# Optimization experiments

Hardware: AMD Instinct MI355X
Metric: run time of the kernel (lower is better)

The kernel has to match this reference:

```python
import jax, jax.numpy as jnp
import numpy as np
from jax import lax

WEIGHT_PREC = 8
ACT_PREC = 8
ACT_BOUND = 6.0  # fixed symmetric activation bound (quant_act.bounds)
EPS = 1e-6


def _ste_round(v):
    # AQT round-to-nearest with straight-through estimator
    return v + lax.stop_gradient(jnp.floor(v + 0.5) - v)


def setup_inputs() -> dict:
    key = jax.random.key(0)
    k1, k2 = jax.random.split(key)
    B, D, F = 131072, 512, 512
    x = jax.random.normal(k1, (B, D), dtype=jnp.float32)
    # lecun_normal-style kernel init
    kernel = jax.random.normal(k2, (D, F), dtype=jnp.float32) * (1.0 / np.sqrt(D))
    bias = jnp.zeros((F,), dtype=jnp.float32)
    padding_mask = jnp.ones((B, 1), dtype=bool)
    return {"x": x, "kernel": kernel, "bias": bias, "padding_mask": padding_mask}


def reference(x, kernel, bias, padding_mask):
    # padding_mask only affects bounds statistics collection; with fixed act
    # bounds and train=False it does not enter the math.
    wmax = float(2 ** (WEIGHT_PREC - 1) - 1)  # 127
    amax = float(2 ** (ACT_PREC - 1) - 1)     # 127

    # per-channel weight quantization: axis=(0,), scale shape (1, features)
    w_bound = jnp.maximum(jnp.max(jnp.abs(kernel), axis=0, keepdims=True), EPS)
    w_scale = wmax / w_bound                   # (1, F)
    w_q = jnp.clip(_ste_round(kernel * w_scale), -wmax, wmax)

    # per-tensor symmetric activation quantization with fixed bound
    a_scale = amax / ACT_BOUND                 # scalar
    x_q = jnp.clip(_ste_round(x * a_scale), -amax, amax)

    # integer-valued dot_general, then dequantize by the combined scale
    y = jnp.einsum('bd,df->bf', x_q, w_q)      # [B, F]
    y = y / (a_scale * w_scale)                # broadcast (1, F)
    return y + bias[jnp.newaxis, :]
```

## Files before the change

kernel.cpp:

```cpp
#include <hip/hip_runtime.h>
#include <stdint.h>

typedef int   int32x4   __attribute__((ext_vector_type(4)));
typedef int   int32x16  __attribute__((ext_vector_type(16)));
typedef float floatx4   __attribute__((ext_vector_type(4)));

#define B_ROWS 131072
#define DK 512
#define FN 512
#define A_SCALE_F ((float)(127.0 / 6.0))

#define GBLK 256
#define GT   512
#define BMS  32
#define GTILES (B_ROWS / BMS / GBLK)

__global__ void wq_quant_kernel(const float* __restrict__ kern,
                                int8_t* __restrict__ wq,
                                float* __restrict__ invcs) {
  __shared__ float smax[256];
  __shared__ float sscale[4];
  const int c = threadIdx.x & 3;
  const int g = threadIdx.x >> 2;
  const int col = blockIdx.x * 4 + c;

  float m = 0.f;
#pragma unroll
  for (int i = 0; i < 8; ++i) {
    m = fmaxf(m, fabsf(kern[(size_t)(g * 8 + i) * FN + col]));
  }
  smax[threadIdx.x] = m;
  __syncthreads();
  if (threadIdx.x < 4) {
    float mm = smax[threadIdx.x];
#pragma unroll 8
    for (int g2 = 1; g2 < 64; ++g2) mm = fmaxf(mm, smax[g2 * 4 + threadIdx.x]);
    const float wb = fmaxf(mm, 1e-6f);
    const float ws = 127.f / wb;
    sscale[threadIdx.x] = ws;
    invcs[blockIdx.x * 4 + threadIdx.x] =
        (float)(1.0 / ((double)A_SCALE_F * (double)ws));
  }
  __syncthreads();
  const float ws = sscale[c];
  uint32_t* wq32 = (uint32_t*)(wq + (size_t)col * DK);
#pragma unroll
  for (int d = 0; d < 2; ++d) {
    uint32_t p = 0;
#pragma unroll
    for (int j = 0; j < 4; ++j) {
      float v = kern[(size_t)(g * 8 + d * 4 + j) * FN + col] * ws;
      v = floorf(v + 0.5f);
      v = fminf(fmaxf(v, -127.f), 127.f);
      p |= ((uint32_t)((int)v & 255)) << (8 * j);
    }
    wq32[g * 2 + d] = p;
  }
}

__device__ __forceinline__ uint32_t quant4(floatx4 v) {
  uint32_t p = 0;
#pragma unroll
  for (int j = 0; j < 4; ++j) {
    float q = floorf(v[j] * A_SCALE_F + 0.5f);
    q = fminf(fmaxf(q, -127.f), 127.f);
    p |= ((uint32_t)((int)q & 255)) << (8 * j);
  }
  return p;
}

__global__ __launch_bounds__(GT, 2)
void aqt_gemm_fused(const float* __restrict__ x,
                    const int8_t* __restrict__ wq,
                    const float* __restrict__ invcs,
                    const float* __restrict__ bias,
                    float* __restrict__ out) {
  __shared__ __align__(16) uint8_t xq[2][BMS * DK];

  const int tid  = threadIdx.x;
  const int lane = tid & 63;
  const int wv   = tid >> 6;
  const int l31  = lane & 31;
  const int l5   = lane >> 5;

  const int c4 = tid & 127;
  const int rg = tid >> 7;

  const int col0 = wv * 64 + l31;
  const int col1 = col0 + 32;
  int32x4 Bf0[16], Bf1[16];
#pragma unroll
  for (int ks = 0; ks < 16; ++ks) {
    Bf0[ks] = *(const int32x4*)(wq + (size_t)col0 * DK + ks * 32 + l5 * 16);
    Bf1[ks] = *(const int32x4*)(wq + (size_t)col1 * DK + ks * 32 + l5 * 16);
  }
  const float inv0 = invcs[col0], bv0 = bias[col0];
  const float inv1 = invcs[col1], bv1 = bias[col1];

  const size_t row0 = (size_t)blockIdx.x * (GTILES * BMS);

#define LOADV(vdst, rt)                                                       \
  {                                                                           \
    const float* xg_ = x + (size_t)(rt) * DK;                                 \
    _Pragma("unroll")                                                         \
    for (int i_ = 0; i_ < 8; ++i_)                                            \
      vdst[i_] = *(const floatx4*)(xg_ + (size_t)(i_ * 4 + rg) * DK + c4 * 4);\
  }

#define QWRITE(vsrc, bufp)                                                    \
  {                                                                           \
    _Pragma("unroll")                                                         \
    for (int i_ = 0; i_ < 8; ++i_) {                                          \
      const int r_ = i_ * 4 + rg;                                             \
      *(uint32_t*)(&(bufp)[r_ * DK + ((c4 * 4) ^ ((r_ & 31) << 4))]) =        \
          quant4(vsrc[i_]);                                                   \
    }                                                                         \
  }

#define PANEL(Bf, colv, invv, bvv, bufp, rt)                                  \
  {                                                                           \
    int32x16 acc = (int32x16)(0);                                             \
    const uint8_t* aRow_ = (bufp) + l31 * DK;                                 \
    _Pragma("unroll")                                                         \
    for (int ks_ = 0; ks_ < 16; ++ks_) {                                      \
      int32x4 a_ = *(const int32x4*)(aRow_ + ((ks_ * 32 + l5 * 16) ^ (l31 << 4))); \
      acc = __builtin_amdgcn_mfma_i32_32x32x32_i8(a_, Bf[ks_], acc, 0, 0, 0); \
    }                                                                         \
    _Pragma("unroll")                                                         \
    for (int r_ = 0; r_ < 16; ++r_) {                                         \
      const int rowl_ = (r_ & 3) + 8 * (r_ >> 2) + 4 * l5;                    \
      out[((rt) + rowl_) * FN + (colv)] = (float)acc[r_] * (invv) + (bvv);    \
    }                                                                         \
  }

  floatx4 vA[8], vB[8];

  LOADV(vA, row0);
  QWRITE(vA, (&xq[0][0]));
  LOADV(vB, row0 + BMS);
  asm volatile("s_waitcnt lgkmcnt(0)" ::: "memory");
  __builtin_amdgcn_s_barrier();

#pragma unroll 1
  for (int t = 0; t < GTILES; t += 2) {
    const size_t rowT = row0 + (size_t)t * BMS;

    if (t + 2 < GTILES) LOADV(vA, rowT + 2 * BMS);
    PANEL(Bf0, col0, inv0, bv0, (&xq[0][0]), rowT);
    PANEL(Bf1, col1, inv1, bv1, (&xq[0][0]), rowT);
    QWRITE(vB, (&xq[1][0]));
    asm volatile("s_waitcnt lgkmcnt(0)" ::: "memory");
    __builtin_amdgcn_s_barrier();

    if (t + 3 < GTILES) LOADV(vB, rowT + 3 * BMS);
    PANEL(Bf0, col0, inv0, bv0, (&xq[1][0]), rowT + BMS);
    PANEL(Bf1, col1, inv1, bv1, (&xq[1][0]), rowT + BMS);
    if (t + 2 < GTILES) QWRITE(vA, (&xq[0][0]));
    asm volatile("s_waitcnt lgkmcnt(0)" ::: "memory");
    __builtin_amdgcn_s_barrier();
  }

#undef LOADV
#undef QWRITE
#undef PANEL
}

extern "C" void kernel_launch(void* const* d_in, const int* in_sizes, int n_in,
                              void* d_out, int out_size, void* d_ws, size_t ws_size,
                              hipStream_t stream) {
  const float* x    = (const float*)d_in[0];
  const float* kern = (const float*)d_in[1];
  const float* bias = (const float*)d_in[2];

  int8_t* wq    = (int8_t*)d_ws;
  float*  invcs = (float*)((char*)d_ws + (size_t)FN * DK);

  wq_quant_kernel<<<128, 256, 0, stream>>>(kern, wq, invcs);
  aqt_gemm_fused<<<GBLK, GT, 0, stream>>>(x, wq, invcs, bias, (float*)d_out);
}
```

Measured before the change: 123.3 us.

## Deepen LDS pipeline to four buffers with one barrier per tile pair

Restructures the main loop to use four LDS buffers of quantized activations, processing two tiles per iteration with a single barrier instead of two. Global loads run further ahead, and quantized writes go into the alternate pair of buffers while MFMA panels consume the current pair. It also packs the int8 results with v_perm instructions and uses an fma for the scale plus half. LDS use doubles, which may constrain occupancy, and keeping more loads in flight raises register pressure.

```diff
diff --git a/kernel.cpp b/kernel.cpp
--- a/kernel.cpp
+++ b/kernel.cpp
@@ -59,14 +59,16 @@
 }
 
 __device__ __forceinline__ uint32_t quant4(floatx4 v) {
-  uint32_t p = 0;
+  int32x4 q;
 #pragma unroll
   for (int j = 0; j < 4; ++j) {
-    float q = floorf(v[j] * A_SCALE_F + 0.5f);
-    q = fminf(fmaxf(q, -127.f), 127.f);
-    p |= ((uint32_t)((int)q & 255)) << (8 * j);
+    float f = floorf(fmaf(v[j], A_SCALE_F, 0.5f));
+    f = fminf(fmaxf(f, -127.f), 127.f);
+    q[j] = (int)f;
   }
-  return p;
+  uint32_t w01 = __builtin_amdgcn_perm((uint32_t)q[1], (uint32_t)q[0], 0x00000400u);
+  uint32_t w23 = __builtin_amdgcn_perm((uint32_t)q[3], (uint32_t)q[2], 0x00000400u);
+  return __builtin_amdgcn_perm(w23, w01, 0x05040100u);
 }
 
 __global__ __launch_bounds__(GT, 2)
@@ -75,7 +77,7 @@
                     const float* __restrict__ invcs,
                     const float* __restrict__ bias,
                     float* __restrict__ out) {
-  __shared__ __align__(16) uint8_t xq[2][BMS * DK];
+  __shared__ __align__(16) uint8_t xq[4][BMS * DK];
 
   const int tid  = threadIdx.x;
   const int lane = tid & 63;
@@ -136,26 +138,34 @@
   floatx4 vA[8], vB[8];
 
   LOADV(vA, row0);
+  LOADV(vB, row0 + BMS);
   QWRITE(vA, (&xq[0][0]));
-  LOADV(vB, row0 + BMS);
+  QWRITE(vB, (&xq[1][0]));
+  LOADV(vA, row0 + 2 * BMS);
+  LOADV(vB, row0 + 3 * BMS);
   asm volatile("s_waitcnt lgkmcnt(0)" ::: "memory");
   __builtin_amdgcn_s_barrier();
 
 #pragma unroll 1
-  for (int t = 0; t < GTILES; t += 2) {
-    const size_t rowT = row0 + (size_t)t * BMS;
+  for (int q = 0; q < GTILES / 2; ++q) {
+    const size_t rowT = row0 + (size_t)(2 * q) * BMS;
+    uint8_t* cur0 = &xq[(q & 1) ? 2 : 0][0];
+    uint8_t* cur1 = cur0 + BMS * DK;
+    uint8_t* nxt0 = &xq[(q & 1) ? 0 : 2][0];
+    uint8_t* nxt1 = nxt0 + BMS * DK;
+    const bool hasQ = (q < GTILES / 2 - 1);
+    const bool hasL = (q < GTILES / 2 - 2);
 
-    if (t + 2 < GTILES) LOADV(vA, rowT + 2 * BMS);
-    PANEL(Bf0, col0, inv0, bv0, (&xq[0][0]), rowT);
-    PANEL(Bf1, col1, inv1, bv1, (&xq[0][0]), rowT);
-    QWRITE(vB, (&xq[1][0]));
-    asm volatile("s_waitcnt lgkmcnt(0)" ::: "memory");
-    __builtin_amdgcn_s_barrier();
+    if (hasQ) QWRITE(vA, nxt0);
+    if (hasL) LOADV(vA, rowT + 4 * BMS);
+    PANEL(Bf0, col0, inv0, bv0, cur0, rowT);
+    PANEL(Bf1, col1, inv1, bv1, cur0, rowT);
 
-    if (t + 3 < GTILES) LOADV(vB, rowT + 3 * BMS);
-    PANEL(Bf0, col0, inv0, bv0, (&xq[1][0]), rowT + BMS);
-    PANEL(Bf1, col1, inv1, bv1, (&xq[1][0]), rowT + BMS);
-    if (t + 2 < GTILES) QWRITE(vA, (&xq[0][0]));
+    if (hasQ) QWRITE(vB, nxt1);
+    if (hasL) LOADV(vB, rowT + 5 * BMS);
+    PANEL(Bf0, col0, inv0, bv0, cur1, rowT + BMS);
+    PANEL(Bf1, col1, inv1, bv1, cur1, rowT + BMS);
+
     asm volatile("s_waitcnt lgkmcnt(0)" ::: "memory");
     __builtin_amdgcn_s_barrier();
   }
```

After: 151.2 us. 1.23x slower.
